# Kernel tuning notes

Hardware: AMD Instinct MI355X
Metric: run time of the kernel (lower is better)

Reference implementation:

```python
import jax, jax.numpy as jnp
import numpy as np

NUM_EMBEDDINGS = 512
EMBEDDING_DIM = 64
COMMITMENT_COST = 0.25


def setup_inputs() -> dict:
    key = jax.random.key(0)
    k1, k2 = jax.random.split(key)
    inputs = jax.random.normal(k1, (32, 64, 64, 64), dtype=jnp.float32)  # NCHW
    # nn.Embedding init: uniform(-1/K, 1/K)
    weight = jax.random.uniform(
        k2, (NUM_EMBEDDINGS, EMBEDDING_DIM), dtype=jnp.float32,
        minval=-1.0 / NUM_EMBEDDINGS, maxval=1.0 / NUM_EMBEDDINGS)
    return {"inputs": inputs, "weight": weight}


def reference(inputs, weight):
    # NCHW -> NHWC
    x = jnp.transpose(inputs, (0, 2, 3, 1))
    in_shape = x.shape
    flat = x.reshape(-1, EMBEDDING_DIM)                  # [N, D]
    # squared euclidean distances to each codebook vector: [N, K]
    d = (jnp.sum(flat ** 2, axis=1, keepdims=True)
         + jnp.sum(weight ** 2, axis=1)
         - 2.0 * flat @ weight.T)
    codebook_indices = jnp.argmin(d, axis=1)             # [N] int
    quantized = weight[codebook_indices].reshape(in_shape)  # gather lookup

    e_latent_loss = jnp.mean((jax.lax.stop_gradient(quantized) - x) ** 2)
    q_latent_loss = jnp.mean((quantized - jax.lax.stop_gradient(x)) ** 2)
    loss = q_latent_loss + COMMITMENT_COST * e_latent_loss

    # straight-through estimator
    quantized = x + jax.lax.stop_gradient(quantized - x)

    # perplexity from code usage histogram (equivalent to one-hot mean)
    n = flat.shape[0]
    counts = jnp.zeros((NUM_EMBEDDINGS,), jnp.float32).at[codebook_indices].add(1.0)
    avg_probs = counts / n
    perplexity = jnp.exp(-jnp.sum(avg_probs * jnp.log(avg_probs + 1e-10)))

    quantized_nchw = jnp.transpose(quantized, (0, 3, 1, 2))
    return (loss, quantized_nchw, perplexity, codebook_indices)
```

## Files before the change

kernel.cpp:

```cpp
#include <hip/hip_runtime.h>
#include <math.h>

#define NUM_K   512
#define DIM     64
#define NROWS   131072
#define NELEM   8388608
#define Q_OFF    1
#define PERP_OFF 8388609
#define IDX_OFF  8388610

#define MARGIN  1.0e-4f

typedef short  bf16x8 __attribute__((ext_vector_type(8)));
typedef float  f32x4  __attribute__((ext_vector_type(4)));


__device__ __forceinline__ unsigned short f2bf(float f) {
    unsigned u = __float_as_uint(f);
    return (unsigned short)((u + 0x7FFFu + ((u >> 16) & 1u)) >> 16);
}
__device__ __forceinline__ float bf2f(unsigned short h) {
    return __uint_as_float(((unsigned)h) << 16);
}

__device__ __forceinline__ unsigned long long eval_chain(
        const float* __restrict__ xr, float xsq,
        const float* __restrict__ w, float wsq, int k) {
    const float* wk = w + (size_t)k * DIM;
    float d = 0.f;
#pragma unroll
    for (int c = 0; c < DIM; c += 4) {
        float4 wv = *(const float4*)(wk + c);
        d = fmaf(xr[c + 0], wv.x, d);
        d = fmaf(xr[c + 1], wv.y, d);
        d = fmaf(xr[c + 2], wv.z, d);
        d = fmaf(xr[c + 3], wv.w, d);
    }
    float s = __fsub_rn(__fadd_rn(xsq, wsq), __fmul_rn(2.f, d));
    return ((unsigned long long)__float_as_uint(s) << 32) | (unsigned)k;
}

__global__ __launch_bounds__(256) void vq_prep(const float* __restrict__ w,
                                               float* __restrict__ swsq_g,
                                               unsigned short* __restrict__ wpack) {
    const int id = blockIdx.x * 256 + threadIdx.x;
    if (id < NUM_K) {
        const float* wk = w + id * DIM;
        float r[8];
#pragma unroll
        for (int j = 0; j < 8; ++j) r[j] = __fmul_rn(wk[j], wk[j]);
#pragma unroll
        for (int t = 1; t < 8; ++t)
#pragma unroll
            for (int j = 0; j < 8; ++j)
                r[j] = __fadd_rn(r[j], __fmul_rn(wk[8 * t + j], wk[8 * t + j]));
        swsq_g[id] = __fadd_rn(
            __fadd_rn(__fadd_rn(r[0], r[1]), __fadd_rn(r[2], r[3])),
            __fadd_rn(__fadd_rn(r[4], r[5]), __fadd_rn(r[6], r[7])));
    }
    const int kt = id >> 8, f = (id >> 6) & 3, l = id & 63;
    const int step = f >> 1, pass = f & 1;
    const int coln = kt * 16 + (l & 15), quad = l >> 4;
    const float* src = w + (size_t)coln * DIM + step * 32 + quad * 8;
    unsigned short tmp[8];
#pragma unroll
    for (int j = 0; j < 8; ++j) {
        float v = src[j];
        unsigned short hi = f2bf(v);
        tmp[j] = pass ? f2bf(v - bf2f(hi)) : hi;
    }
    *(uint4*)(wpack + (size_t)id * 8) = *(uint4*)tmp;
}

__global__ __launch_bounds__(256, 3) void vq_phase1(
        const float* __restrict__ x,
        const float* __restrict__ w,
        const float* __restrict__ swsq_g,
        const uint4* __restrict__ wpack,
        float* __restrict__ out_q,
        float* __restrict__ out_idx,
        float* __restrict__ loss_sum,
        unsigned* __restrict__ counts) {
    __shared__ float swsq[NUM_K];
    __shared__ unsigned hcnt[NUM_K];
    __shared__ float xs[128 * 65];
    __shared__ float sxsq[128];
    __shared__ int sidx[128];
    __shared__ float wred[4];
    __shared__ unsigned long long rred[4];
    __shared__ int rlist[128];
    __shared__ int rcount;

    const int tid  = threadIdx.x;
    const int lane = tid & 63;
    const int wvid = tid >> 6;
    const int quad = lane >> 4;
    const int m    = lane & 15;
    const int n0   = blockIdx.x * 128;
    const int b    = n0 >> 12;
    const int hw0  = n0 & 4095;
    const float* xbase = x + (size_t)b * 262144 + hw0;

    if (tid == 0) rcount = 0;
    for (int i = tid; i < NUM_K; i += 256) { swsq[i] = swsq_g[i]; hcnt[i] = 0; }

    bf16x8 afr[2][2][2];
#pragma unroll
    for (int rt = 0; rt < 2; ++rt) {
        const int row = wvid * 32 + rt * 16 + m;
        const float* xp = xbase + row;
#pragma unroll
        for (int s = 0; s < 2; ++s) {
            union { bf16x8 v; unsigned short u[8]; } hi, lo;
#pragma unroll
            for (int j = 0; j < 8; ++j) {
                const int c = s * 32 + quad * 8 + j;
                float v = xp[(size_t)c * 4096];
                xs[row * 65 + c] = v;
                unsigned short h = f2bf(v);
                hi.u[j] = h;
                lo.u[j] = f2bf(v - bf2f(h));
            }
            afr[rt][s][0] = hi.v;
            afr[rt][s][1] = lo.v;
        }
    }
    __syncthreads();

    if (tid < 128) {
        const float* xr = &xs[tid * 65];
        float p0 = 0.f, p1 = 0.f, p2 = 0.f, p3 = 0.f;
#pragma unroll
        for (int c = 0; c < DIM; c += 4) {
            p0 = fmaf(xr[c + 0], xr[c + 0], p0);
            p1 = fmaf(xr[c + 1], xr[c + 1], p1);
            p2 = fmaf(xr[c + 2], xr[c + 2], p2);
            p3 = fmaf(xr[c + 3], xr[c + 3], p3);
        }
        sxsq[tid] = __fadd_rn(__fadd_rn(p0, p1), __fadd_rn(p2, p3));
    }
    __syncthreads();

    float min1[2][4], min2[2][4], min3[2][4]; int idx1[2][4], idx2[2][4];
#pragma unroll
    for (int rt = 0; rt < 2; ++rt)
#pragma unroll
        for (int r = 0; r < 4; ++r) {
            min1[rt][r] = 3.4e38f; min2[rt][r] = 3.4e38f; min3[rt][r] = 3.4e38f;
            idx1[rt][r] = 0; idx2[rt][r] = 0;
        }

    uint4 P[2][4];
    {
        const uint4* t0 = wpack;
        const uint4* t1 = wpack + 256;
#pragma unroll
        for (int q = 0; q < 4; ++q) { P[0][q] = t0[q * 64 + lane];
                                      P[1][q] = t1[q * 64 + lane]; }
    }
#pragma unroll 1
    for (int kt = 0; kt < 32; kt += 2) {
#pragma unroll
        for (int h = 0; h < 2; ++h) {
            bf16x8 bh0 = __builtin_bit_cast(bf16x8, P[h][0]);
            bf16x8 bl0 = __builtin_bit_cast(bf16x8, P[h][1]);
            bf16x8 bh1 = __builtin_bit_cast(bf16x8, P[h][2]);
            bf16x8 bl1 = __builtin_bit_cast(bf16x8, P[h][3]);
            const int kg = (kt + h) * 16 + m;
            const float wsqv = swsq[kg];
            if (kt + h + 2 < 32) {
                const uint4* np = wpack + (size_t)(kt + h + 2) * 256;
#pragma unroll
                for (int q = 0; q < 4; ++q) P[h][q] = np[q * 64 + lane];
            }
#pragma unroll
            for (int rt = 0; rt < 2; ++rt) {
                f32x4 acc = {0.f, 0.f, 0.f, 0.f};
                acc = __builtin_amdgcn_mfma_f32_16x16x32_bf16(afr[rt][0][0], bh0, acc, 0, 0, 0);
                acc = __builtin_amdgcn_mfma_f32_16x16x32_bf16(afr[rt][0][0], bl0, acc, 0, 0, 0);
                acc = __builtin_amdgcn_mfma_f32_16x16x32_bf16(afr[rt][0][1], bh0, acc, 0, 0, 0);
                acc = __builtin_amdgcn_mfma_f32_16x16x32_bf16(afr[rt][1][0], bh1, acc, 0, 0, 0);
                acc = __builtin_amdgcn_mfma_f32_16x16x32_bf16(afr[rt][1][0], bl1, acc, 0, 0, 0);
                acc = __builtin_amdgcn_mfma_f32_16x16x32_bf16(afr[rt][1][1], bh1, acc, 0, 0, 0);
#pragma unroll
                for (int r = 0; r < 4; ++r) {
                    float s = fmaf(-2.f, acc[r], wsqv);
                    bool lt1 = s < min1[rt][r];
                    bool lt2 = s < min2[rt][r];
                    min3[rt][r] = __builtin_amdgcn_fmed3f(min2[rt][r], min3[rt][r], s);
                    idx2[rt][r] = lt1 ? idx1[rt][r] : (lt2 ? kg : idx2[rt][r]);
                    min2[rt][r] = __builtin_amdgcn_fmed3f(min1[rt][r], min2[rt][r], s);
                    idx1[rt][r] = lt1 ? kg : idx1[rt][r];
                    min1[rt][r] = fminf(min1[rt][r], s);
                }
            }
        }
    }

#pragma unroll 1
    for (int rt = 0; rt < 2; ++rt)
#pragma unroll 1
        for (int r = 0; r < 4; ++r) {
            float g1 = min1[rt][r]; int gi = idx1[rt][r];
#pragma unroll
            for (int d = 1; d < 16; d <<= 1) {
                float og = __shfl_xor(g1, d);
                int   oi = __shfl_xor(gi, d);
                if (og < g1) { g1 = og; gi = oi; }
            }
            const float lim = g1 + MARGIN;
            const bool c1 = min1[rt][r] <= lim;
            const bool c2 = min2[rt][r] <= lim;
            const bool f3 = min3[rt][r] <= lim;
            unsigned long long b1 = __ballot(c1);
            unsigned long long b2 = __ballot(c2);
            unsigned long long b3 = __ballot(f3);
            const unsigned fld1 = (unsigned)(b1 >> (quad * 16)) & 0xFFFFu;
            const unsigned fld2 = (unsigned)(b2 >> (quad * 16)) & 0xFFFFu;
            const unsigned fld3 = (unsigned)(b3 >> (quad * 16)) & 0xFFFFu;
            const int  nc   = __popc(fld1) + __popc(fld2);
            const bool flag = fld3 != 0;
            const int rowL = wvid * 32 + rt * 16 + quad * 4 + r;
            unsigned long long best = ~0ull;
            if (!flag && nc > 1) {
                const float* xr = &xs[rowL * 65];
                const float xq = sxsq[rowL];
                const int k1 = c1 ? idx1[rt][r] : idx2[rt][r];
                if (c1 || c2) best = eval_chain(xr, xq, w, swsq[k1], k1);
                if (c1 && c2) {
                    unsigned long long e =
                        eval_chain(xr, xq, w, swsq[idx2[rt][r]], idx2[rt][r]);
                    best = e < best ? e : best;
                }
            }
#pragma unroll
            for (int d = 1; d < 16; d <<= 1) {
                unsigned long long o = __shfl_xor(best, d);
                best = o < best ? o : best;
            }
            if (m == 0) {
                if (flag) rlist[atomicAdd(&rcount, 1)] = rowL;
                else sidx[rowL] = (nc > 1) ? (int)(best & 0xFFFFFFFFull) : gi;
            }
        }
    __syncthreads();

    const int rc = rcount;
#pragma unroll 1
    for (int i = 0; i < rc; ++i) {
        const int rowL = rlist[i];
        const float* xr = &xs[rowL * 65];
        const float xq = sxsq[rowL];
        unsigned long long bb = eval_chain(xr, xq, w, swsq[tid], tid);
        unsigned long long e2 = eval_chain(xr, xq, w, swsq[tid + 256], tid + 256);
        if (e2 < bb) bb = e2;
#pragma unroll
        for (int d = 1; d < 64; d <<= 1) {
            unsigned long long o = __shfl_xor(bb, d);
            if (o < bb) bb = o;
        }
        if (lane == 0) rred[wvid] = bb;
        __syncthreads();
        if (tid == 0) {
            unsigned long long q0 = rred[0] < rred[1] ? rred[0] : rred[1];
            unsigned long long q1 = rred[2] < rred[3] ? rred[2] : rred[3];
            sidx[rowL] = (int)((q0 < q1 ? q0 : q1) & 0xFFFFFFFFull);
        }
        __syncthreads();
    }

    {
        const int rb = tid & 127, cg = tid >> 7;
        const int bk = sidx[rb];
        const float* xr = &xs[rb * 65];
        float dsum = 0.f;
        const float4* wb = (const float4*)(w + (size_t)bk * DIM + cg * 32);
        float* oq = out_q + (size_t)b * 262144 + hw0 + rb;
        if (cg == 0) {
            out_idx[n0 + rb] = (float)bk;
            atomicAdd(&hcnt[bk], 1u);
        }
#pragma unroll
        for (int j4 = 0; j4 < 8; ++j4) {
            float4 v = wb[j4];
            const int c = cg * 32 + j4 * 4;
            float e0 = v.x - xr[c + 0];
            float e1 = v.y - xr[c + 1];
            float e2 = v.z - xr[c + 2];
            float e3 = v.w - xr[c + 3];
            dsum = fmaf(e0, e0, dsum);
            dsum = fmaf(e1, e1, dsum);
            dsum = fmaf(e2, e2, dsum);
            dsum = fmaf(e3, e3, dsum);
            oq[(size_t)(c + 0) * 4096] = v.x;
            oq[(size_t)(c + 1) * 4096] = v.y;
            oq[(size_t)(c + 2) * 4096] = v.z;
            oq[(size_t)(c + 3) * 4096] = v.w;
        }
#pragma unroll
        for (int off = 32; off > 0; off >>= 1) dsum += __shfl_down(dsum, off);
        if (lane == 0) wred[wvid] = dsum;
    }
    __syncthreads();
    if (tid == 0)
        atomicAdd(loss_sum, (wred[0] + wred[1]) + (wred[2] + wred[3]));
    for (int i = tid; i < NUM_K; i += 256) {
        unsigned cc = hcnt[i];
        if (cc) atomicAdd(&counts[i], cc);
    }
}

__global__ __launch_bounds__(512) void vq_final(
        const unsigned* __restrict__ counts,
        const float* __restrict__ loss_sum,
        float* __restrict__ out) {
    __shared__ float red[8];
    const int tid = threadIdx.x;
    float p = (float)counts[tid] * (1.f / (float)NROWS);
    float t = p * logf(p + 1e-10f);
#pragma unroll
    for (int off = 32; off > 0; off >>= 1) t += __shfl_down(t, off);
    if ((tid & 63) == 0) red[tid >> 6] = t;
    __syncthreads();
    if (tid == 0) {
        float s = 0.f;
#pragma unroll
        for (int i = 0; i < 8; ++i) s += red[i];
        out[PERP_OFF] = expf(-s);
        out[0] = loss_sum[0] * (1.25f / (float)NELEM);
    }
}

extern "C" void kernel_launch(void* const* d_in, const int* in_sizes, int n_in,
                              void* d_out, int out_size, void* d_ws, size_t ws_size,
                              hipStream_t stream) {
    const float* x = (const float*)d_in[0];
    const float* w = (const float*)d_in[1];
    float* out = (float*)d_out;
    char* ws = (char*)d_ws;
    float*    loss_sum = (float*)ws;
    unsigned* counts   = (unsigned*)(ws + 16);
    float*    swsq_g   = (float*)(ws + 4096);
    unsigned short* wpack = (unsigned short*)(ws + 8192);

    hipMemsetAsync(d_ws, 0, 2064, stream);

    vq_prep<<<32, 256, 0, stream>>>(w, swsq_g, wpack);
    vq_phase1<<<NROWS / 128, 256, 0, stream>>>(x, w, swsq_g, (const uint4*)wpack,
                                               out + Q_OFF, out + IDX_OFF,
                                               loss_sum, counts);
    vq_final<<<1, 512, 0, stream>>>(counts, loss_sum, out);
}
```

Baseline: 161.1 us.

## Pack codebook index into distance bits, replicate histograms, fuse final reduction

```diff
diff --git a/kernel.cpp b/kernel.cpp
--- a/kernel.cpp
+++ b/kernel.cpp
@@ -9,7 +9,7 @@
 #define PERP_OFF 8388609
 #define IDX_OFF  8388610
 
-#define MARGIN  1.0e-4f
+#define MARGIN  1.7e-4f
 
 typedef short  bf16x8 __attribute__((ext_vector_type(8)));
 typedef float  f32x4  __attribute__((ext_vector_type(4)));
@@ -42,8 +42,14 @@
 
 __global__ __launch_bounds__(256) void vq_prep(const float* __restrict__ w,
                                                float* __restrict__ swsq_g,
-                                               unsigned short* __restrict__ wpack) {
+                                               unsigned short* __restrict__ wpack,
+                                               unsigned* __restrict__ counts,
+                                               int rep_words,
+                                               float* __restrict__ loss_sum,
+                                               unsigned* __restrict__ ticket) {
     const int id = blockIdx.x * 256 + threadIdx.x;
+    if (id < rep_words) counts[id] = 0u;
+    if (id == 0) { loss_sum[0] = 0.f; ticket[0] = 0u; }
     if (id < NUM_K) {
         const float* wk = w + id * DIM;
         float r[8];
@@ -77,10 +83,11 @@
         const float* __restrict__ w,
         const float* __restrict__ swsq_g,
         const uint4* __restrict__ wpack,
-        float* __restrict__ out_q,
-        float* __restrict__ out_idx,
+        float* __restrict__ out,
         float* __restrict__ loss_sum,
-        unsigned* __restrict__ counts) {
+        unsigned* __restrict__ counts,
+        unsigned* __restrict__ ticket,
+        int rep_mask) {
     __shared__ float swsq[NUM_K];
     __shared__ unsigned hcnt[NUM_K];
     __shared__ float xs[128 * 65];
@@ -90,6 +97,8 @@
     __shared__ unsigned long long rred[4];
     __shared__ int rlist[128];
     __shared__ int rcount;
+    __shared__ unsigned s_tick;
+    __shared__ float red8[8];
 
     const int tid  = threadIdx.x;
     const int lane = tid & 63;
@@ -100,6 +109,8 @@
     const int b    = n0 >> 12;
     const int hw0  = n0 & 4095;
     const float* xbase = x + (size_t)b * 262144 + hw0;
+    float* out_q   = out + Q_OFF;
+    float* out_idx = out + IDX_OFF;
 
     if (tid == 0) rcount = 0;
     for (int i = tid; i < NUM_K; i += 256) { swsq[i] = swsq_g[i]; hcnt[i] = 0; }
@@ -141,13 +152,12 @@
     }
     __syncthreads();
 
-    float min1[2][4], min2[2][4], min3[2][4]; int idx1[2][4], idx2[2][4];
+    float m1v[2][4], m2v[2][4], m3v[2][4];
 #pragma unroll
     for (int rt = 0; rt < 2; ++rt)
 #pragma unroll
         for (int r = 0; r < 4; ++r) {
-            min1[rt][r] = 3.4e38f; min2[rt][r] = 3.4e38f; min3[rt][r] = 3.4e38f;
-            idx1[rt][r] = 0; idx2[rt][r] = 0;
+            m1v[rt][r] = 3.4e38f; m2v[rt][r] = 3.4e38f; m3v[rt][r] = 3.4e38f;
         }
 
     uint4 P[2][4];
@@ -184,34 +194,38 @@
                 acc = __builtin_amdgcn_mfma_f32_16x16x32_bf16(afr[rt][1][1], bh1, acc, 0, 0, 0);
 #pragma unroll
                 for (int r = 0; r < 4; ++r) {
-                    float s = fmaf(-2.f, acc[r], wsqv);
-                    bool lt1 = s < min1[rt][r];
-                    bool lt2 = s < min2[rt][r];
-                    min3[rt][r] = __builtin_amdgcn_fmed3f(min2[rt][r], min3[rt][r], s);
-                    idx2[rt][r] = lt1 ? idx1[rt][r] : (lt2 ? kg : idx2[rt][r]);
-                    min2[rt][r] = __builtin_amdgcn_fmed3f(min1[rt][r], min2[rt][r], s);
-                    idx1[rt][r] = lt1 ? kg : idx1[rt][r];
-                    min1[rt][r] = fminf(min1[rt][r], s);
+                    float s  = fmaf(-2.f, acc[r], wsqv);
+                    float sp = __uint_as_float(
+                        (__float_as_uint(s) & 0xFFFFFE00u) | (unsigned)kg);
+                    m3v[rt][r] = __builtin_amdgcn_fmed3f(m2v[rt][r], m3v[rt][r], sp);
+                    m2v[rt][r] = __builtin_amdgcn_fmed3f(m1v[rt][r], m2v[rt][r], sp);
+                    m1v[rt][r] = fminf(m1v[rt][r], sp);
                 }
             }
         }
     }
 
-#pragma unroll 1
+    float gm[2][4];
+#pragma unroll
     for (int rt = 0; rt < 2; ++rt)
-#pragma unroll 1
+#pragma unroll
         for (int r = 0; r < 4; ++r) {
-            float g1 = min1[rt][r]; int gi = idx1[rt][r];
-#pragma unroll
-            for (int d = 1; d < 16; d <<= 1) {
-                float og = __shfl_xor(g1, d);
-                int   oi = __shfl_xor(gi, d);
-                if (og < g1) { g1 = og; gi = oi; }
-            }
-            const float lim = g1 + MARGIN;
-            const bool c1 = min1[rt][r] <= lim;
-            const bool c2 = min2[rt][r] <= lim;
-            const bool f3 = min3[rt][r] <= lim;
+            float g = m1v[rt][r];
+            g = fminf(g, __shfl_xor(g, 1));
+            g = fminf(g, __shfl_xor(g, 2));
+            g = fminf(g, __shfl_xor(g, 4));
+            g = fminf(g, __shfl_xor(g, 8));
+            gm[rt][r] = g;
+        }
+
+#pragma unroll 1
+    for (int rt = 0; rt < 2; ++rt)
+#pragma unroll 1
+        for (int r = 0; r < 4; ++r) {
+            const float lim = gm[rt][r] + MARGIN;
+            const bool c1 = m1v[rt][r] <= lim;
+            const bool c2 = m2v[rt][r] <= lim;
+            const bool f3 = m3v[rt][r] <= lim;
             unsigned long long b1 = __ballot(c1);
             unsigned long long b2 = __ballot(c2);
             unsigned long long b3 = __ballot(f3);
@@ -225,11 +239,13 @@
             if (!flag && nc > 1) {
                 const float* xr = &xs[rowL * 65];
                 const float xq = sxsq[rowL];
-                const int k1 = c1 ? idx1[rt][r] : idx2[rt][r];
-                if (c1 || c2) best = eval_chain(xr, xq, w, swsq[k1], k1);
-                if (c1 && c2) {
-                    unsigned long long e =
-                        eval_chain(xr, xq, w, swsq[idx2[rt][r]], idx2[rt][r]);
+                if (c1) {
+                    const int ka = (int)(__float_as_uint(m1v[rt][r]) & 511u);
+                    best = eval_chain(xr, xq, w, swsq[ka], ka);
+                }
+                if (c2) {
+                    const int kb = (int)(__float_as_uint(m2v[rt][r]) & 511u);
+                    unsigned long long e = eval_chain(xr, xq, w, swsq[kb], kb);
                     best = e < best ? e : best;
                 }
             }
@@ -240,7 +256,9 @@
             }
             if (m == 0) {
                 if (flag) rlist[atomicAdd(&rcount, 1)] = rowL;
-                else sidx[rowL] = (nc > 1) ? (int)(best & 0xFFFFFFFFull) : gi;
+                else sidx[rowL] = (nc > 1)
+                        ? (int)(best & 0xFFFFFFFFull)
+                        : (int)(__float_as_uint(gm[rt][r]) & 511u);
             }
         }
     __syncthreads();
@@ -304,30 +322,39 @@
     __syncthreads();
     if (tid == 0)
         atomicAdd(loss_sum, (wred[0] + wred[1]) + (wred[2] + wred[3]));
-    for (int i = tid; i < NUM_K; i += 256) {
-        unsigned cc = hcnt[i];
-        if (cc) atomicAdd(&counts[i], cc);
-    }
-}
-
-__global__ __launch_bounds__(512) void vq_final(
-        const unsigned* __restrict__ counts,
-        const float* __restrict__ loss_sum,
-        float* __restrict__ out) {
-    __shared__ float red[8];
-    const int tid = threadIdx.x;
-    float p = (float)counts[tid] * (1.f / (float)NROWS);
-    float t = p * logf(p + 1e-10f);
-#pragma unroll
-    for (int off = 32; off > 0; off >>= 1) t += __shfl_down(t, off);
-    if ((tid & 63) == 0) red[tid >> 6] = t;
-    __syncthreads();
-    if (tid == 0) {
-        float s = 0.f;
-#pragma unroll
-        for (int i = 0; i < 8; ++i) s += red[i];
-        out[PERP_OFF] = expf(-s);
-        out[0] = loss_sum[0] * (1.25f / (float)NELEM);
+    {
+        unsigned* mycnt = counts + ((blockIdx.x & rep_mask) << 9);
+        for (int i = tid; i < NUM_K; i += 256) {
+            unsigned cc = hcnt[i];
+            if (cc) atomicAdd(&mycnt[i], cc);
+        }
+    }
+
+    __syncthreads();
+    if (tid == 0) s_tick = atomicAdd(ticket, 1u);
+    __syncthreads();
+    if (s_tick == (unsigned)(gridDim.x - 1)) {
+#pragma unroll 1
+        for (int half = 0; half < 2; ++half) {
+            const int k = (wvid + half * 4) * 64 + lane;
+            unsigned cnt = 0;
+            for (int rr = 0; rr <= rep_mask; ++rr)
+                cnt += atomicAdd(&counts[(rr << 9) + k], 0u);
+            float p = (float)cnt * (1.f / (float)NROWS);
+            float t = p * logf(p + 1e-10f);
+#pragma unroll
+            for (int off = 32; off > 0; off >>= 1) t += __shfl_down(t, off);
+            if (lane == 0) red8[wvid + half * 4] = t;
+        }
+        __syncthreads();
+        if (tid == 0) {
+            float s = 0.f;
+#pragma unroll
+            for (int i = 0; i < 8; ++i) s += red8[i];
+            out[PERP_OFF] = expf(-s);
+            float ls = atomicAdd(loss_sum, 0.f);
+            out[0] = ls * (1.25f / (float)NELEM);
+        }
     }
 }
 
@@ -338,16 +365,20 @@
     const float* w = (const float*)d_in[1];
     float* out = (float*)d_out;
     char* ws = (char*)d_ws;
+
+    int rep = 16;
+    while (rep > 2 && (size_t)(64 + rep * 2048 + 2048 + 131072) > ws_size)
+        rep >>= 1;
+
     float*    loss_sum = (float*)ws;
-    unsigned* counts   = (unsigned*)(ws + 16);
-    float*    swsq_g   = (float*)(ws + 4096);
-    unsigned short* wpack = (unsigned short*)(ws + 8192);
-
-    hipMemsetAsync(d_ws, 0, 2064, stream);
-
-    vq_prep<<<32, 256, 0, stream>>>(w, swsq_g, wpack);
+    unsigned* ticket   = (unsigned*)(ws + 8);
+    unsigned* counts   = (unsigned*)(ws + 64);
+    float*    swsq_g   = (float*)(ws + 64 + rep * 2048);
+    unsigned short* wpack = (unsigned short*)(ws + 64 + rep * 2048 + 2048);
+
+    vq_prep<<<32, 256, 0, stream>>>(w, swsq_g, wpack, counts, rep * 512,
+                                    loss_sum, ticket);
     vq_phase1<<<NROWS / 128, 256, 0, stream>>>(x, w, swsq_g, (const uint4*)wpack,
-                                               out + Q_OFF, out + IDX_OFF,
-                                               loss_sum, counts);
-    vq_final<<<1, 512, 0, stream>>>(counts, loss_sum, out);
-}
+                                               out, loss_sum, counts, ticket,
+                                               rep - 1);
+}
```

Measured after the change: 152.0 us. 1.06x faster.
